# Optimization experiments

Hardware: AMD Instinct MI355X
Metric: run time of the kernel (lower is better)

Reference implementation:

```python
import jax, jax.numpy as jnp
import numpy as np

B, N, DIM, HEADS, DIM_HEAD, DEPTH = 2, 2048, 1024, 16, 64, 2
DIM_COND = DIM * 4
DIM_INNER_FF = int(DIM * 4 * 2 / 3)  # 2730, GEGLU inner dim
SOFTCAP = 50.0
SCALE = DIM_HEAD ** -0.5
TWO_PI = 2.0 * np.pi


def l2norm(x):
    n = jnp.sqrt(jnp.sum(x * x, axis=-1, keepdims=True))
    return x / jnp.maximum(n, 1e-12)


def rmsnorm(x, gamma):
    return l2norm(x) * (DIM ** 0.5) * (gamma + 1.0)


def layernorm(x):
    mu = jnp.mean(x, axis=-1, keepdims=True)
    var = jnp.mean(jnp.square(x - mu), axis=-1, keepdims=True)
    return (x - mu) * jax.lax.rsqrt(var + 1e-5)


def rotate_half(x):
    # interleaved-pair rotation (rotary_embedding_torch convention)
    p = x.reshape(x.shape[:-1] + (-1, 2))
    a, b = p[..., 0], p[..., 1]
    return jnp.stack((-b, a), axis=-1).reshape(x.shape)


def forward(x, times, rotary_emb, fourier_weights, time_w, time_b,
            attn_film_w, attn_film_b, attn_adazero_w, attn_adazero_b,
            attn_ln_gamma, attn_layerscale, attn_rms_gamma, w_qkv, w_out,
            ff_film_w, ff_film_b, ff_adazero_w, ff_adazero_b,
            ff_ln_gamma, ff_layerscale, ff_rms_gamma, ff_w1, ff_b1, ff_w2, ff_b2,
            final_rms_gamma, modality_positions):
    # time conditioning: RandomFourierEmbed -> Linear -> SiLU  -> [b, n, 4*dim]
    fr = times[..., None] * fourier_weights * TWO_PI
    fourier = jnp.concatenate([times[..., None], jnp.sin(fr), jnp.cos(fr)], axis=-1)
    cond = jax.nn.silu(fourier @ time_w + time_b)

    # masks from modality spans (type, offset, length)
    seq = jnp.arange(N)
    offsets = modality_positions[..., 1]
    lengths = modality_positions[..., 2]
    in_q = seq[None, None, :] >= offsets[..., None]              # [b, m, n]
    in_k = seq[None, None, :] < (offsets + lengths)[..., None]   # [b, m, n]
    causal = seq[:, None] >= seq[None, :]
    attn_mask = causal[None] | jnp.any(in_q[..., :, None] & in_k[..., None, :], axis=1)  # [b, i, j]
    is_any_modality = jnp.any(in_q & in_k, axis=1)[..., None]    # [b, n, 1]
    neg = -jnp.finfo(x.dtype).max
    cosf = jnp.cos(rotary_emb)
    sinf = jnp.sin(rotary_emb)

    def adaptive(x_in, film_w, film_b, az_w, az_b, ln_g, lscale, fn):
        h = layernorm(x_in)
        gamma, beta = jnp.split(cond @ film_w + film_b, 2, axis=-1)
        h = jnp.where(is_any_modality, h * (gamma + 1.0) + beta, h * (ln_g + 1.0))
        out = fn(h)
        gate = jax.nn.sigmoid(cond @ az_w + az_b)
        return jnp.where(is_any_modality, out * gate, out * (lscale + 1.0))

    def attend(h, rms_g, wqkv, wo):
        h = rmsnorm(h, rms_g)
        qkv = (h @ wqkv).reshape(B, N, 3, HEADS, DIM_HEAD)
        q, k, v = jnp.moveaxis(qkv, 2, 0)
        q, k, v = (jnp.swapaxes(t, 1, 2) for t in (q, k, v))  # [b, h, n, d]
        q = q * cosf + rotate_half(q) * sinf
        k = k * cosf + rotate_half(k) * sinf
        sim = jnp.einsum('bhid,bhjd->bhij', q * SCALE, k)
        sim = jnp.tanh(sim / SOFTCAP) * SOFTCAP
        sim = jnp.where(attn_mask[:, None], sim, neg)
        attn = jax.nn.softmax(sim, axis=-1)
        o = jnp.einsum('bhij,bhjd->bhid', attn, v)
        return jnp.swapaxes(o, 1, 2).reshape(B, N, HEADS * DIM_HEAD) @ wo

    def layer(xc, p):
        (afw, afb, azw, azb, alng, als, armsg, wqkv, wo,
         ffw, ffb, fzw, fzb, flng, fls, frmsg, w1, b1, w2, b2) = p
        xc = xc + adaptive(xc, afw, afb, azw, azb, alng, als,
                           lambda h: attend(h, armsg, wqkv, wo))
        def ff(h):
            h = rmsnorm(h, frmsg)
            u, g = jnp.split(h @ w1 + b1, 2, axis=-1)
            return (jax.nn.gelu(g, approximate=False) * u) @ w2 + b2
        xc = xc + adaptive(xc, ffw, ffb, fzw, fzb, flng, fls, ff)
        return xc, None

    stacked = (attn_film_w, attn_film_b, attn_adazero_w, attn_adazero_b,
               attn_ln_gamma, attn_layerscale, attn_rms_gamma, w_qkv, w_out,
               ff_film_w, ff_film_b, ff_adazero_w, ff_adazero_b,
               ff_ln_gamma, ff_layerscale, ff_rms_gamma, ff_w1, ff_b1, ff_w2, ff_b2)
    x, _ = jax.lax.scan(layer, x, stacked)
    return rmsnorm(x, final_rms_gamma)


def setup_inputs():
    key = jax.random.key(0)
    ks = iter(jax.random.split(key, 40))
    def nrm(shape, s=0.02):
        return jax.random.normal(next(ks), shape, dtype=jnp.float32) * s
    L = DEPTH
    inp = {}
    inp['x'] = jax.random.normal(next(ks), (B, N, DIM), dtype=jnp.float32)
    inp['times'] = jax.random.uniform(next(ks), (B, N), dtype=jnp.float32)
    inv_freq = 1.0 / (10000.0 ** (np.arange(0, DIM_HEAD, 2) / DIM_HEAD))
    freqs = np.arange(N)[:, None] * inv_freq[None, :]
    inp['rotary_emb'] = jnp.asarray(np.repeat(freqs, 2, axis=-1), dtype=jnp.float32)
    inp['fourier_weights'] = jax.random.normal(next(ks), (DIM // 2,), dtype=jnp.float32)
    inp['time_w'] = nrm((DIM + 1, DIM_COND))
    inp['time_b'] = nrm((DIM_COND,))
    inp['attn_film_w'] = nrm((L, DIM_COND, 2 * DIM))
    inp['attn_film_b'] = nrm((L, 2 * DIM))
    inp['attn_adazero_w'] = nrm((L, DIM_COND, DIM))
    inp['attn_adazero_b'] = nrm((L, DIM)) - 2.0
    inp['attn_ln_gamma'] = nrm((L, DIM))
    inp['attn_layerscale'] = nrm((L, DIM))
    inp['attn_rms_gamma'] = nrm((L, DIM))
    inp['w_qkv'] = nrm((L, DIM, 3 * HEADS * DIM_HEAD))
    inp['w_out'] = nrm((L, HEADS * DIM_HEAD, DIM))
    inp['ff_film_w'] = nrm((L, DIM_COND, 2 * DIM))
    inp['ff_film_b'] = nrm((L, 2 * DIM))
    inp['ff_adazero_w'] = nrm((L, DIM_COND, DIM))
    inp['ff_adazero_b'] = nrm((L, DIM)) - 2.0
    inp['ff_ln_gamma'] = nrm((L, DIM))
    inp['ff_layerscale'] = nrm((L, DIM))
    inp['ff_rms_gamma'] = nrm((L, DIM))
    inp['ff_w1'] = nrm((L, DIM, 2 * DIM_INNER_FF))
    inp['ff_b1'] = nrm((L, 2 * DIM_INNER_FF))
    inp['ff_w2'] = nrm((L, DIM_INNER_FF, DIM))
    inp['ff_b2'] = nrm((L, DIM))
    inp['final_rms_gamma'] = nrm((DIM,))
    inp['modality_positions'] = jnp.asarray(
        [[[0, 128, 384], [0, 900, 512]],
         [[0, 64, 256], [0, 1200, 600]]], dtype=jnp.int32)
    return inp


def reference(x, times, rotary_emb, fourier_weights, time_w, time_b,
              attn_film_w, attn_film_b, attn_adazero_w, attn_adazero_b,
              attn_ln_gamma, attn_layerscale, attn_rms_gamma, w_qkv, w_out,
              ff_film_w, ff_film_b, ff_adazero_w, ff_adazero_b,
              ff_ln_gamma, ff_layerscale, ff_rms_gamma, ff_w1, ff_b1, ff_w2, ff_b2,
              final_rms_gamma, modality_positions):
    return forward(x, times, rotary_emb, fourier_weights, time_w, time_b,
                   attn_film_w, attn_film_b, attn_adazero_w, attn_adazero_b,
                   attn_ln_gamma, attn_layerscale, attn_rms_gamma, w_qkv, w_out,
                   ff_film_w, ff_film_b, ff_adazero_w, ff_adazero_b,
                   ff_ln_gamma, ff_layerscale, ff_rms_gamma, ff_w1, ff_b1, ff_w2, ff_b2,
                   final_rms_gamma, modality_positions)
```

## Files before the change

### kernel.cpp

```cpp
#include <hip/hip_runtime.h>
#include <math.h>

#define B_      2
#define N_      2048
#define DIM_    1024
#define ROWS_   4096
#define DCOND_  4096
#define DFF_    2730
#define DFF1_   5460
#define KF_     1056
#define KM_     2752
#define NGL_    5504
#define SCALE_  0.125f
#define TWO_PI_ 6.28318530717958647692f

#define KSTR_   72
#define VSTR_   72
#define PSTR_   68

typedef __attribute__((ext_vector_type(8))) short bfx8;
typedef __attribute__((ext_vector_type(4))) float fx4;

__device__ __forceinline__ float b2f(unsigned short u) {
  return __uint_as_float(((unsigned)u) << 16);
}
__device__ __forceinline__ unsigned short f2b(float f) {
  unsigned x = __float_as_uint(f);
  return (unsigned short)((x + 0x7FFF + ((x >> 16) & 1)) >> 16);
}

__device__ __forceinline__ bool tile_active(const int* mp, int bm) {
  int bb = bm >> 11;
  int r0 = bm & 2047, r1 = r0 + 128;
  int o0 = mp[bb * 6 + 1], e0 = o0 + mp[bb * 6 + 2];
  int o1 = mp[bb * 6 + 4], e1 = o1 + mp[bb * 6 + 5];
  return ((o0 < e0) && (r0 < e0) && (r1 > o0)) ||
         ((o1 < e1) && (r0 < e1) && (r1 > o1));
}

template <int CTRL>
__device__ __forceinline__ float dppf(float v) {
  return __uint_as_float((unsigned)__builtin_amdgcn_update_dpp(
      0, (int)__float_as_uint(v), CTRL, 0xf, 0xf, true));
}
__device__ __forceinline__ float rowmax16(float v) {
  v = fmaxf(v, dppf<0x121>(v));
  v = fmaxf(v, dppf<0x122>(v));
  v = fmaxf(v, dppf<0x124>(v));
  v = fmaxf(v, dppf<0x128>(v));
  return v;
}
__device__ __forceinline__ float rowsum16(float v) {
  v += dppf<0x121>(v);
  v += dppf<0x122>(v);
  v += dppf<0x124>(v);
  v += dppf<0x128>(v);
  return v;
}

__global__ __launch_bounds__(256) void fourier_kernel(const float* __restrict__ times,
                                                      const float* __restrict__ fw,
                                                      const int* __restrict__ mp,
                                                      unsigned short* __restrict__ F) {
  int r = blockIdx.x;
  if (!tile_active(mp, r & ~127)) return;
  float tv = times[r];
  unsigned short* Fr = F + (size_t)r * KF_;
  for (int c = threadIdx.x; c < KF_; c += 256) {
    float v;
    if (c == 0)          v = tv;
    else if (c <= 512)   v = sinf(tv * fw[c - 1] * TWO_PI_);
    else if (c <= 1024)  v = cosf(tv * fw[c - 513] * TWO_PI_);
    else                 v = 0.f;
    Fr[c] = f2b(v);
  }
}

__global__ __launch_bounds__(256) void transpose_w(const float* __restrict__ W,
                                                   unsigned short* __restrict__ WT,
                                                   int K, int N, int KP) {
  __shared__ float t[32][33];
  int tx = threadIdx.x, ty = threadIdx.y;
  int k0 = blockIdx.x * 32, n0 = blockIdx.y * 32;
#pragma unroll
  for (int i = 0; i < 4; ++i) {
    int k = k0 + ty + i * 8, n = n0 + tx;
    t[ty + i * 8][tx] = (k < K && n < N) ? W[(size_t)k * N + n] : 0.f;
  }
  __syncthreads();
#pragma unroll
  for (int i = 0; i < 4; ++i) {
    int n = n0 + ty + i * 8;
    if (n < N) WT[(size_t)n * KP + k0 + tx] = f2b(t[tx][ty + i * 8]);
  }
}

__global__ __launch_bounds__(256) void transpose_w_geglu(const float* __restrict__ W,
                                                         unsigned short* __restrict__ WT) {
  __shared__ float t[32][33];
  int tx = threadIdx.x, ty = threadIdx.y;
  int k0 = blockIdx.x * 32;
  int n0 = blockIdx.y * 32;
  int group = n0 >> 5;
  int ucol = group * 16 + (tx & 15);
  int src = (tx < 16) ? ucol : (DFF_ + ucol);
  bool valid = ucol < DFF_;
#pragma unroll
  for (int i = 0; i < 4; ++i) {
    int k = k0 + ty + i * 8;
    t[ty + i * 8][tx] = valid ? W[(size_t)k * DFF1_ + src] : 0.f;
  }
  __syncthreads();
#pragma unroll
  for (int i = 0; i < 4; ++i) {
    int n = n0 + ty + i * 8;
    WT[(size_t)n * 1024 + k0 + tx] = f2b(t[tx][ty + i * 8]);
  }
}

__global__ __launch_bounds__(256) void vtrans_kernel(const unsigned short* __restrict__ QKV,
                                                     unsigned short* __restrict__ VT) {
  __shared__ unsigned short t[32][33];
  int bh = blockIdx.z;
  int b = bh >> 4, h = bh & 15;
  int n0 = blockIdx.x * 32, d0 = blockIdx.y * 32;
  int tx = threadIdx.x, ty = threadIdx.y;
#pragma unroll
  for (int i = 0; i < 4; ++i) {
    int n = n0 + ty + i * 8;
    t[ty + i * 8][tx] = QKV[(size_t)(b * N_ + n) * 3072 + 2048 + h * 64 + d0 + tx];
  }
  __syncthreads();
#pragma unroll
  for (int i = 0; i < 4; ++i) {
    int d = d0 + ty + i * 8;
    VT[((size_t)bh * 64 + d) * N_ + n0 + tx] = t[tx][ty + i * 8];
  }
}

__global__ __launch_bounds__(256) void mfma_gemm(const unsigned short* __restrict__ A,
                                                 const unsigned short* __restrict__ BT,
                                                 const float* __restrict__ bias,
                                                 const float* __restrict__ bias2,
                                                 void* __restrict__ Cout,
                                                 void* __restrict__ Cout2,
                                                 const int* __restrict__ skip,
                                                 int K, int Nc, int mode, int out_bf) {
  __shared__ unsigned short As[128 * 32];
  __shared__ unsigned short Bs[128 * 32];
  int tid = threadIdx.x;
  int wave = tid >> 6, lane = tid & 63;
  int bm = blockIdx.y * 128, bn = blockIdx.x * 128;
  if (skip && !tile_active(skip, bm)) return;
  int wm = (wave >> 1) * 64, wn = (wave & 1) * 64;
  int lr = lane >> 4, lc = lane & 15;
  fx4 acc[4][4];
#pragma unroll
  for (int i = 0; i < 4; ++i)
#pragma unroll
    for (int j = 0; j < 4; ++j) acc[i][j] = (fx4){0.f, 0.f, 0.f, 0.f};

  for (int k0 = 0; k0 < K; k0 += 32) {
#pragma unroll
    for (int i = 0; i < 2; ++i) {
      int c = tid + i * 256;
      int row = c >> 2, kc = (c & 3) * 8;
      __builtin_amdgcn_global_load_lds(
          (const __attribute__((address_space(1))) void*)(A + (size_t)(bm + row) * K + k0 + kc),
          (__attribute__((address_space(3))) void*)(&As[c * 8]), 16, 0, 0);
      __builtin_amdgcn_global_load_lds(
          (const __attribute__((address_space(1))) void*)(BT + (size_t)(bn + row) * K + k0 + kc),
          (__attribute__((address_space(3))) void*)(&Bs[c * 8]), 16, 0, 0);
    }
    __syncthreads();
    bfx8 af[4], bf[4];
#pragma unroll
    for (int mi = 0; mi < 4; ++mi)
      af[mi] = *(const bfx8*)&As[(wm + mi * 16 + lc) * 32 + lr * 8];
#pragma unroll
    for (int ni = 0; ni < 4; ++ni)
      bf[ni] = *(const bfx8*)&Bs[(wn + ni * 16 + lc) * 32 + lr * 8];
    __builtin_amdgcn_s_setprio(1);
#pragma unroll
    for (int mi = 0; mi < 4; ++mi)
#pragma unroll
      for (int ni = 0; ni < 4; ++ni)
        acc[mi][ni] = __builtin_amdgcn_mfma_f32_16x16x32_bf16(af[mi], bf[ni], acc[mi][ni], 0, 0, 0);
    __builtin_amdgcn_s_setprio(0);
    __syncthreads();
  }

  if (mode == 5) {
#pragma unroll
    for (int mi = 0; mi < 4; ++mi)
#pragma unroll
      for (int ni = 0; ni < 4; ni += 2) {
        int colu = bn + wn + ni * 16 + lc;
        int mc = (colu >> 5) * 16 + lc;
        bool valid = mc < DFF_;
        float bu = valid ? bias[mc] : 0.f;
        float bg = valid ? bias[DFF_ + mc] : 0.f;
#pragma unroll
        for (int r = 0; r < 4; ++r) {
          int row = bm + wm + mi * 16 + lr * 4 + r;
          float u = acc[mi][ni][r] + bu;
          float gg = acc[mi][ni + 1][r] + bg;
          float ge = 0.5f * gg * (1.f + erff(gg * 0.70710678118654752440f));
          ((unsigned short*)Cout)[(size_t)row * KM_ + mc] = f2b(valid ? ge * u : 0.f);
        }
      }
    return;
  }
  if (mode == 4) {
#pragma unroll
    for (int mi = 0; mi < 4; ++mi)
#pragma unroll
      for (int ni = 0; ni < 4; ++ni) {
        int col = bn + wn + ni * 16 + lc;
        if (col < 2048) {
          float bv = bias[col];
#pragma unroll
          for (int r = 0; r < 4; ++r) {
            int row = bm + wm + mi * 16 + lr * 4 + r;
            ((float*)Cout)[(size_t)row * 2048 + col] = acc[mi][ni][r] + bv;
          }
        } else {
          int c2 = col - 2048;
          float bv = bias2[c2];
#pragma unroll
          for (int r = 0; r < 4; ++r) {
            int row = bm + wm + mi * 16 + lr * 4 + r;
            float v = acc[mi][ni][r] + bv;
            ((float*)Cout2)[(size_t)row * 1024 + c2] = 1.f / (1.f + __expf(-v));
          }
        }
      }
    return;
  }
#pragma unroll
  for (int mi = 0; mi < 4; ++mi) {
#pragma unroll
    for (int ni = 0; ni < 4; ++ni) {
      int col = bn + wn + ni * 16 + lc;
      if (col >= Nc) continue;
      float bv = (mode >= 1) ? bias[col] : 0.f;
#pragma unroll
      for (int r = 0; r < 4; ++r) {
        int row = bm + wm + mi * 16 + lr * 4 + r;
        float v = acc[mi][ni][r] + bv;
        if (mode == 2)      v = v / (1.f + __expf(-v));
        else if (mode == 3) v = 1.f / (1.f + __expf(-v));
        if (out_bf) ((unsigned short*)Cout)[(size_t)row * Nc + col] = f2b(v);
        else        ((float*)Cout)[(size_t)row * Nc + col] = v;
      }
    }
  }
}

__global__ __launch_bounds__(256) void ismod_kernel(const int* __restrict__ mp,
                                                    float* __restrict__ ismod) {
  int idx = blockIdx.x * 256 + threadIdx.x;
  int b = idx >> 11, n = idx & 2047;
  const int* p = mp + b * 6;
  bool m = false;
#pragma unroll
  for (int mi = 0; mi < 2; ++mi) {
    int off = p[mi * 3 + 1], len = p[mi * 3 + 2];
    m = m || ((n >= off) && (n < off + len));
  }
  ismod[idx] = m ? 1.f : 0.f;
}

__global__ __launch_bounds__(256) void fuse_pre_kernel(
    float* __restrict__ X, const float* __restrict__ O,
    const float* __restrict__ grs,
    const float* __restrict__ ls,
    const float* __restrict__ film,
    const float* __restrict__ lng,
    const float* __restrict__ rg,
    const float* __restrict__ ismod,
    unsigned short* __restrict__ Yb) {
  int r = blockIdx.x, tid = threadIdx.x;
  bool im = ismod[r] != 0.f;
  float xv[4];
  float s = 0.f, ss = 0.f;
#pragma unroll
  for (int k = 0; k < 4; ++k) {
    int c = tid + k * 256;
    size_t idx = (size_t)r * 1024 + c;
    float x = X[idx];
    if (grs) {
      float ov = O[idx];
      x += im ? ov * grs[idx] : ov * (ls[c] + 1.f);
      X[idx] = x;
    }
    xv[k] = x; s += x; ss += x * x;
  }
#pragma unroll
  for (int o = 32; o > 0; o >>= 1) { s += __shfl_down(s, o); ss += __shfl_down(ss, o); }
  __shared__ float shs[4], shss[4], sh2[4];
  int w = tid >> 6;
  if ((tid & 63) == 0) { shs[w] = s; shss[w] = ss; }
  __syncthreads();
  float mu = (shs[0] + shs[1] + shs[2] + shs[3]) * (1.f / DIM_);
  float var = (shss[0] + shss[1] + shss[2] + shss[3]) * (1.f / DIM_) - mu * mu;
  float rstd = rsqrtf(var + 1e-5f);
  float h[4]; float s2 = 0.f;
#pragma unroll
  for (int k = 0; k < 4; ++k) {
    int c = tid + k * 256;
    float hh = (xv[k] - mu) * rstd;
    hh = im ? hh * (film[(size_t)r * 2048 + c] + 1.f) + film[(size_t)r * 2048 + 1024 + c]
            : hh * (lng[c] + 1.f);
    h[k] = hh; s2 += hh * hh;
  }
#pragma unroll
  for (int o = 32; o > 0; o >>= 1) s2 += __shfl_down(s2, o);
  if ((tid & 63) == 0) sh2[w] = s2;
  __syncthreads();
  float tot = sh2[0] + sh2[1] + sh2[2] + sh2[3];
  float scale = 32.f / fmaxf(sqrtf(tot), 1e-12f);
#pragma unroll
  for (int k = 0; k < 4; ++k) {
    int c = tid + k * 256;
    Yb[(size_t)r * 1024 + c] = f2b(h[k] * scale * (rg[c] + 1.f));
  }
}

__global__ __launch_bounds__(256) void rms_final_kernel(
    const float* __restrict__ X, const float* __restrict__ O,
    const float* __restrict__ grs, const float* __restrict__ ls,
    const float* __restrict__ ismod, const float* __restrict__ g,
    float* __restrict__ out) {
  int r = blockIdx.x, tid = threadIdx.x;
  bool im = ismod[r] != 0.f;
  float xv[4]; float ss = 0.f;
#pragma unroll
  for (int k = 0; k < 4; ++k) {
    int c = tid + k * 256;
    size_t idx = (size_t)r * 1024 + c;
    float ov = O[idx];
    float x = X[idx] + (im ? ov * grs[idx] : ov * (ls[c] + 1.f));
    xv[k] = x; ss += x * x;
  }
#pragma unroll
  for (int o = 32; o > 0; o >>= 1) ss += __shfl_down(ss, o);
  __shared__ float shss[4];
  int w = tid >> 6;
  if ((tid & 63) == 0) shss[w] = ss;
  __syncthreads();
  float tots = shss[0] + shss[1] + shss[2] + shss[3];
  float scale = 32.f / fmaxf(sqrtf(tots), 1e-12f);
#pragma unroll
  for (int k = 0; k < 4; ++k) {
    int c = tid + k * 256;
    out[(size_t)r * 1024 + c] = xv[k] * scale * (g[c] + 1.f);
  }
}

__global__ __launch_bounds__(256) void ropetab_kernel(const float* __restrict__ rot,
                                                      float* __restrict__ tab) {
  int i = blockIdx.x * 256 + threadIdx.x;
  float f = rot[i];
  tab[2 * i]     = cosf(f);
  tab[2 * i + 1] = sinf(f);
}

__global__ __launch_bounds__(256) void rotary_kernel(unsigned short* __restrict__ QKV,
                                                     const float* __restrict__ tab) {
  int idx = blockIdx.x * 256 + threadIdx.x;
  int r = idx >> 10;
  int c0 = (idx & 1023) * 2;
  float2 t2 = ((const float2*)tab)[(r & 2047) * 64 + (c0 & 63)];
  float cs = t2.x, sn = t2.y;
  unsigned* p = (unsigned*)(QKV + (size_t)r * 3072 + c0);
  unsigned v = *p;
  float x0 = b2f((unsigned short)(v & 0xFFFF));
  float x1 = b2f((unsigned short)(v >> 16));
  float y0 = x0 * cs - x1 * sn;
  float y1 = x1 * cs + x0 * sn;
  *p = (unsigned)f2b(y0) | ((unsigned)f2b(y1) << 16);
}

__global__ __launch_bounds__(256) void attn_kernel(const unsigned short* __restrict__ QKV,
                                                   const unsigned short* __restrict__ VTg,
                                                   const int* __restrict__ mp,
                                                   unsigned short* __restrict__ O) {
  __shared__ unsigned short Ks[64 * KSTR_];
  __shared__ unsigned short Vt[64 * VSTR_];
  __shared__ unsigned short Ps[4][16 * PSTR_];
  int bh = blockIdx.y;
  int b = bh >> 4, h = bh & 15;
  int qb = 31 - blockIdx.x;
  int tid = threadIdx.x, wave = tid >> 6, lane = tid & 63;
  int lg = lane >> 4, ln = lane & 15;
  int off0 = mp[b * 6 + 1], end0 = off0 + mp[b * 6 + 2];
  int off1 = mp[b * 6 + 4], end1 = off1 + mp[b * 6 + 5];
  int qmin = qb * 64;
  int qmax = qmin + 63;

  int qrow = qb * 64 + wave * 16 + ln;
  bfx8 qf0 = *(const bfx8*)(QKV + (size_t)(b * N_ + qrow) * 3072 + h * 64 + lg * 8);
  bfx8 qf1 = *(const bfx8*)(QKV + (size_t)(b * N_ + qrow) * 3072 + h * 64 + 32 + lg * 8);

  fx4 od[4];
#pragma unroll
  for (int i = 0; i < 4; ++i) od[i] = (fx4){0.f, 0.f, 0.f, 0.f};
  float m_[4] = {-3.0e38f, -3.0e38f, -3.0e38f, -3.0e38f};
  float l_[4] = {0.f, 0.f, 0.f, 0.f};
  int ibase = qb * 64 + wave * 16 + lg * 4;

  for (int jt = 0; jt < 32; ++jt) {
    int j0 = jt * 64;
    if (!((j0 <= qmax) || (qmax >= off0 && j0 < end0) || (qmax >= off1 && j0 < end1))) continue;
    bool full = (j0 + 63 <= qmin) || (qmin >= off0 && j0 + 63 < end0)
             || (qmin >= off1 && j0 + 63 < end1);
    __syncthreads();
    for (int e = tid; e < 512; e += 256) {
      int jj = e >> 3, dc = (e & 7) * 8;
      *(bfx8*)&Ks[jj * KSTR_ + dc] =
          *(const bfx8*)(QKV + (size_t)(b * N_ + j0 + jj) * 3072 + 1024 + h * 64 + dc);
    }
    for (int e = tid; e < 512; e += 256) {
      int d = e >> 3, kc = (e & 7) * 8;
      *(bfx8*)&Vt[d * VSTR_ + kc] =
          *(const bfx8*)(VTg + ((size_t)bh * 64 + d) * N_ + j0 + kc);
    }
    __syncthreads();
    fx4 sf[4];
    __builtin_amdgcn_s_setprio(1);
#pragma unroll
    for (int kn = 0; kn < 4; ++kn) {
      fx4 a = (fx4){0.f, 0.f, 0.f, 0.f};
      bfx8 b0 = *(const bfx8*)&Ks[(kn * 16 + ln) * KSTR_ + lg * 8];
      bfx8 b1 = *(const bfx8*)&Ks[(kn * 16 + ln) * KSTR_ + 32 + lg * 8];
      a = __builtin_amdgcn_mfma_f32_16x16x32_bf16(qf0, b0, a, 0, 0, 0);
      a = __builtin_amdgcn_mfma_f32_16x16x32_bf16(qf1, b1, a, 0, 0, 0);
      sf[kn] = a;
    }
    __builtin_amdgcn_s_setprio(0);
    float sv[4][4];
#pragma unroll
    for (int kn = 0; kn < 4; ++kn)
#pragma unroll
      for (int reg = 0; reg < 4; ++reg) {
        float e2 = __expf(sf[kn][reg] * 0.005f);
        float r = __builtin_amdgcn_rcpf(e2 + 1.f);
        sv[kn][reg] = fmaf(-100.f, r, 50.f);
      }
    if (!full) {
#pragma unroll
      for (int kn = 0; kn < 4; ++kn) {
        int j = j0 + kn * 16 + ln;
#pragma unroll
        for (int reg = 0; reg < 4; ++reg) {
          int i = ibase + reg;
          bool ok = (i >= j) || (i >= off0 && j < end0) || (i >= off1 && j < end1);
          sv[kn][reg] = ok ? sv[kn][reg] : -1.0e30f;
        }
      }
    }
    float scl[4];
#pragma unroll
    for (int reg = 0; reg < 4; ++reg) {
      float tm = fmaxf(fmaxf(sv[0][reg], sv[1][reg]), fmaxf(sv[2][reg], sv[3][reg]));
      tm = rowmax16(tm);
      float mn = fmaxf(m_[reg], tm);
      scl[reg] = __expf(m_[reg] - mn);
      m_[reg] = mn;
    }
    float ts[4];
#pragma unroll
    for (int reg = 0; reg < 4; ++reg) {
      float t = 0.f;
#pragma unroll
      for (int kn = 0; kn < 4; ++kn) {
        float pp = __expf(sv[kn][reg] - m_[reg]);
        sv[kn][reg] = pp;
        t += pp;
      }
      ts[reg] = rowsum16(t);
    }
#pragma unroll
    for (int reg = 0; reg < 4; ++reg) l_[reg] = l_[reg] * scl[reg] + ts[reg];
#pragma unroll
    for (int kn = 0; kn < 4; ++kn)
#pragma unroll
      for (int reg = 0; reg < 4; ++reg)
        Ps[wave][(lg * 4 + reg) * PSTR_ + kn * 16 + ln] = f2b(sv[kn][reg]);
#pragma unroll
    for (int dn = 0; dn < 4; ++dn)
#pragma unroll
      for (int reg = 0; reg < 4; ++reg) od[dn][reg] *= scl[reg];
    bfx8 pf0 = *(const bfx8*)&Ps[wave][ln * PSTR_ + lg * 8];
    bfx8 pf1 = *(const bfx8*)&Ps[wave][ln * PSTR_ + 32 + lg * 8];
    __builtin_amdgcn_s_setprio(1);
#pragma unroll
    for (int dn = 0; dn < 4; ++dn) {
      bfx8 v0 = *(const bfx8*)&Vt[(dn * 16 + ln) * VSTR_ + lg * 8];
      bfx8 v1 = *(const bfx8*)&Vt[(dn * 16 + ln) * VSTR_ + 32 + lg * 8];
      od[dn] = __builtin_amdgcn_mfma_f32_16x16x32_bf16(pf0, v0, od[dn], 0, 0, 0);
      od[dn] = __builtin_amdgcn_mfma_f32_16x16x32_bf16(pf1, v1, od[dn], 0, 0, 0);
    }
    __builtin_amdgcn_s_setprio(0);
  }
#pragma unroll
  for (int reg = 0; reg < 4; ++reg) {
    float inv = 1.f / l_[reg];
    unsigned short* orow = O + (size_t)(b * N_ + ibase + reg) * 1024 + h * 64;
#pragma unroll
    for (int dn = 0; dn < 4; ++dn)
      orow[dn * 16 + ln] = f2b(od[dn][reg] * inv);
  }
}

extern "C" void kernel_launch(void* const* d_in, const int* in_sizes, int n_in,
                              void* d_out, int out_size, void* d_ws, size_t ws_size,
                              hipStream_t stream) {
  const float* in_x   = (const float*)d_in[0];
  const float* times  = (const float*)d_in[1];
  const float* rotary = (const float*)d_in[2];
  const float* fwgt   = (const float*)d_in[3];
  const float* time_w = (const float*)d_in[4];
  const float* time_b = (const float*)d_in[5];
  const float* afw    = (const float*)d_in[6];
  const float* afb    = (const float*)d_in[7];
  const float* azw    = (const float*)d_in[8];
  const float* azb    = (const float*)d_in[9];
  const float* alng   = (const float*)d_in[10];
  const float* als    = (const float*)d_in[11];
  const float* armsg  = (const float*)d_in[12];
  const float* wqkv   = (const float*)d_in[13];
  const float* wout   = (const float*)d_in[14];
  const float* ffw    = (const float*)d_in[15];
  const float* ffb    = (const float*)d_in[16];
  const float* fzw    = (const float*)d_in[17];
  const float* fzb    = (const float*)d_in[18];
  const float* flng   = (const float*)d_in[19];
  const float* fls    = (const float*)d_in[20];
  const float* frmsg  = (const float*)d_in[21];
  const float* fw1    = (const float*)d_in[22];
  const float* fb1    = (const float*)d_in[23];
  const float* fw2    = (const float*)d_in[24];
  const float* fb2    = (const float*)d_in[25];
  const float* fing   = (const float*)d_in[26];
  const int*   mp     = (const int*)d_in[27];
  float* out = (float*)d_out;

  char* p = (char*)d_ws;
  unsigned short* wT   = (unsigned short*)p;      p += 25165824;
  float* f_x           = (float*)p;               p += 16777216;
  float* f_o           = (float*)p;               p += 16777216;
  unsigned short* cond = (unsigned short*)p;      p += 33554432;
  unsigned short* hbf  = (unsigned short*)p;      p += 8388608;
  float* film          = (float*)p;               p += 33554432;
  float* gateA         = (float*)p;               p += 16777216;
  float* gateF         = (float*)p;               p += 16777216;
  float* ropetab       = (float*)p;               p += 1048576;
  char* arena          = p;                       p += 41943040;
  float* f_ismod       = (float*)p;               p += 16384;

  unsigned short* qkv    = (unsigned short*)arena;
  unsigned short* vtg    = (unsigned short*)(arena + 25165824);
  unsigned short* attno  = (unsigned short*)(arena + 33554432);
  unsigned short* mid    = (unsigned short*)arena;
  unsigned short* four   = (unsigned short*)arena;

  auto gemm = [&](const unsigned short* A, const float* bias, const float* bias2,
                  void* C, void* C2, const int* skip, int K, int Nc, int mode,
                  int out_bf, int mtiles) {
    mfma_gemm<<<dim3((Nc + 127) / 128, mtiles), 256, 0, stream>>>(
        A, wT, bias, bias2, C, C2, skip, K, Nc, mode, out_bf);
  };
  auto transp = [&](const float* W, unsigned short* dst, int K, int N, int KP) {
    transpose_w<<<dim3(KP / 32, (N + 31) / 32), dim3(32, 8), 0, stream>>>(W, dst, K, N, KP);
  };

  fourier_kernel<<<ROWS_, 256, 0, stream>>>(times, fwgt, mp, four);
  transp(time_w, wT, 1025, DCOND_, KF_);
  gemm(four, time_b, nullptr, cond, nullptr, mp, KF_, DCOND_, 2, 1, 32);
  ismod_kernel<<<ROWS_ / 256, 256, 0, stream>>>(mp, f_ismod);
  ropetab_kernel<<<(2048 * 64) / 256, 256, 0, stream>>>(rotary, ropetab);
  hipMemcpyAsync(f_x, in_x, (size_t)ROWS_ * DIM_ * sizeof(float),
                 hipMemcpyDeviceToDevice, stream);

  for (int l = 0; l < 2; ++l) {
    transp(afw + (size_t)l * DCOND_ * 2048, wT, DCOND_, 2048, DCOND_);
    transp(azw + (size_t)l * DCOND_ * 1024, wT + (size_t)2048 * DCOND_, DCOND_, 1024, DCOND_);
    gemm(cond, afb + l * 2048, azb + l * 1024, film, gateA, mp, DCOND_, 3072, 4, 0, 32);
    fuse_pre_kernel<<<ROWS_, 256, 0, stream>>>(
        f_x, f_o, (l > 0) ? gateF : nullptr, fls + (l - 1) * 1024,
        film, alng + l * 1024, armsg + l * 1024, f_ismod, hbf);
    transp(wqkv + (size_t)l * 1024 * 3072, wT, 1024, 3072, 1024);
    gemm(hbf, nullptr, nullptr, qkv, nullptr, nullptr, 1024, 3072, 0, 1, 32);
    rotary_kernel<<<(ROWS_ * 1024) / 256, 256, 0, stream>>>(qkv, ropetab);
    vtrans_kernel<<<dim3(64, 2, 32), dim3(32, 8), 0, stream>>>(qkv, vtg);
    attn_kernel<<<dim3(32, 32), 256, 0, stream>>>(qkv, vtg, mp, attno);
    transp(wout + (size_t)l * 1024 * 1024, wT, 1024, 1024, 1024);
    gemm(attno, nullptr, nullptr, f_o, nullptr, nullptr, 1024, 1024, 0, 0, 32);

    transp(ffw + (size_t)l * DCOND_ * 2048, wT, DCOND_, 2048, DCOND_);
    transp(fzw + (size_t)l * DCOND_ * 1024, wT + (size_t)2048 * DCOND_, DCOND_, 1024, DCOND_);
    gemm(cond, ffb + l * 2048, fzb + l * 1024, film, gateF, mp, DCOND_, 3072, 4, 0, 32);
    fuse_pre_kernel<<<ROWS_, 256, 0, stream>>>(
        f_x, f_o, gateA, als + l * 1024,
        film, flng + l * 1024, frmsg + l * 1024, f_ismod, hbf);
    transpose_w_geglu<<<dim3(32, NGL_ / 32), dim3(32, 8), 0, stream>>>(
        fw1 + (size_t)l * 1024 * DFF1_, wT);
    gemm(hbf, fb1 + l * DFF1_, nullptr, mid, nullptr, nullptr, 1024, NGL_, 5, 0, 32);
    transp(fw2 + (size_t)l * DFF_ * 1024, wT, DFF_, 1024, KM_);
    gemm(mid, fb2 + l * 1024, nullptr, f_o, nullptr, nullptr, KM_, 1024, 1, 0, 32);
  }

  rms_final_kernel<<<ROWS_, 256, 0, stream>>>(
      f_x, f_o, gateF, fls + 1024, f_ismod, fing, out);
}
```

Baseline: 1.652 ms.

## Prefetch next K/V tile into registers during attention compute

The attention kernel now builds a bitmask of active key tiles up front and walks it with ctz. The next tile's K and V are loaded from global memory into registers while the current tile's MFMA and softmax work runs, then stored to LDS at the top of the next iteration. This hides global-load latency behind compute, at the cost of extra registers per thread, which could lower occupancy.

```diff
diff --git a/kernel.cpp b/kernel.cpp
--- a/kernel.cpp
+++ b/kernel.cpp
@@ -403,6 +403,23 @@
   bfx8 qf0 = *(const bfx8*)(QKV + (size_t)(b * N_ + qrow) * 3072 + h * 64 + lg * 8);
   bfx8 qf1 = *(const bfx8*)(QKV + (size_t)(b * N_ + qrow) * 3072 + h * 64 + 32 + lg * 8);
 
+  int e0 = tid, e1 = tid + 256;
+  const unsigned short* Kp0 = QKV + (size_t)(b * N_ + (e0 >> 3)) * 3072 + 1024 + h * 64 + (e0 & 7) * 8;
+  const unsigned short* Kp1 = QKV + (size_t)(b * N_ + (e1 >> 3)) * 3072 + 1024 + h * 64 + (e1 & 7) * 8;
+  const unsigned short* Vp0 = VTg + ((size_t)bh * 64 + (e0 >> 3)) * N_ + (e0 & 7) * 8;
+  const unsigned short* Vp1 = VTg + ((size_t)bh * 64 + (e1 >> 3)) * N_ + (e1 & 7) * 8;
+  unsigned short* Kd0 = &Ks[(e0 >> 3) * KSTR_ + (e0 & 7) * 8];
+  unsigned short* Kd1 = &Ks[(e1 >> 3) * KSTR_ + (e1 & 7) * 8];
+  unsigned short* Vd0 = &Vt[(e0 >> 3) * VSTR_ + (e0 & 7) * 8];
+  unsigned short* Vd1 = &Vt[(e1 >> 3) * VSTR_ + (e1 & 7) * 8];
+
+  unsigned actmask = 0;
+  for (int t = 0; t < 32; ++t) {
+    int j0 = t * 64;
+    bool act = (j0 <= qmax) || (qmax >= off0 && j0 < end0) || (qmax >= off1 && j0 < end1);
+    actmask |= act ? (1u << t) : 0u;
+  }
+
   fx4 od[4];
 #pragma unroll
   for (int i = 0; i < 4; ++i) od[i] = (fx4){0.f, 0.f, 0.f, 0.f};
@@ -410,23 +427,29 @@
   float l_[4] = {0.f, 0.f, 0.f, 0.f};
   int ibase = qb * 64 + wave * 16 + lg * 4;
 
-  for (int jt = 0; jt < 32; ++jt) {
-    int j0 = jt * 64;
-    if (!((j0 <= qmax) || (qmax >= off0 && j0 < end0) || (qmax >= off1 && j0 < end1))) continue;
+  int jt = __builtin_ctz(actmask);
+  bfx8 kr0 = *(const bfx8*)(Kp0 + (size_t)(jt * 64) * 3072);
+  bfx8 kr1 = *(const bfx8*)(Kp1 + (size_t)(jt * 64) * 3072);
+  bfx8 vr0 = *(const bfx8*)(Vp0 + jt * 64);
+  bfx8 vr1 = *(const bfx8*)(Vp1 + jt * 64);
+
+  while (true) {
+    int cur = jt;
+    actmask &= actmask - 1;
+    int nxt = actmask ? __builtin_ctz(actmask) : -1;
+    int j0 = cur * 64;
     bool full = (j0 + 63 <= qmin) || (qmin >= off0 && j0 + 63 < end0)
              || (qmin >= off1 && j0 + 63 < end1);
     __syncthreads();
-    for (int e = tid; e < 512; e += 256) {
-      int jj = e >> 3, dc = (e & 7) * 8;
-      *(bfx8*)&Ks[jj * KSTR_ + dc] =
-          *(const bfx8*)(QKV + (size_t)(b * N_ + j0 + jj) * 3072 + 1024 + h * 64 + dc);
-    }
-    for (int e = tid; e < 512; e += 256) {
-      int d = e >> 3, kc = (e & 7) * 8;
-      *(bfx8*)&Vt[d * VSTR_ + kc] =
-          *(const bfx8*)(VTg + ((size_t)bh * 64 + d) * N_ + j0 + kc);
-    }
+    *(bfx8*)Kd0 = kr0; *(bfx8*)Kd1 = kr1;
+    *(bfx8*)Vd0 = vr0; *(bfx8*)Vd1 = vr1;
     __syncthreads();
+    if (nxt >= 0) {
+      kr0 = *(const bfx8*)(Kp0 + (size_t)(nxt * 64) * 3072);
+      kr1 = *(const bfx8*)(Kp1 + (size_t)(nxt * 64) * 3072);
+      vr0 = *(const bfx8*)(Vp0 + nxt * 64);
+      vr1 = *(const bfx8*)(Vp1 + nxt * 64);
+    }
     fx4 sf[4];
     __builtin_amdgcn_s_setprio(1);
 #pragma unroll
@@ -503,6 +526,8 @@
       od[dn] = __builtin_amdgcn_mfma_f32_16x16x32_bf16(pf1, v1, od[dn], 0, 0, 0);
     }
     __builtin_amdgcn_s_setprio(0);
+    if (nxt < 0) break;
+    jt = nxt;
   }
 #pragma unroll
   for (int reg = 0; reg < 4; ++reg) {
```

New measurement: 1.627 ms. No clear change (-1.5%).
